# Optimization experiments

Measured on AMD Instinct MI355X. Metric: run time of the kernel, lower is better.

## Reference

```python
import jax, jax.numpy as jnp
import numpy as np
from jax.scipy.special import gammainc

ALPH = 0.8  # significance level (default arg in original forward)


def _median_width(X, iu, ju):
    # pairwise squared distances; original takes median of strictly-positive
    # strict-upper-triangle entries (tril subtracted) -> median over triu(k=1)
    G = jnp.sum(X * X, axis=1)                    # [n]
    D = G[:, None] + G[None, :] - 2.0 * (X @ X.T)  # [n, n]
    du = D[iu, ju]                                 # strict upper triangle, static size
    return jnp.sqrt(0.5 * jnp.median(du))


def _rbf(X, width):
    G = jnp.sum(X * X, axis=1)
    D = G[:, None] + G[None, :] - 2.0 * (X @ X.T)
    return jnp.exp(-D / (2.0 * width ** 2))


def _center(K):
    # H K H with H = I - 11^T/n  ==  K - rowmean - colmean + totalmean
    cm = jnp.mean(K, axis=0, keepdims=True)   # mean over rows  -> [1, n]
    rm = jnp.mean(K, axis=1, keepdims=True)   # mean over cols  -> [n, 1]
    tm = jnp.mean(K)
    return K - cm - rm + tm


def _gamma_ppf(a, p):
    # invert regularized lower incomplete gamma via fixed-iteration bisection
    hi0 = a + 10.0 * jnp.sqrt(a) + 100.0
    def body(i, lohi):
        lo, hi = lohi
        mid = 0.5 * (lo + hi)
        below = gammainc(a, mid) < p
        return (jnp.where(below, mid, lo), jnp.where(below, hi, mid))
    lo, hi = jax.lax.fori_loop(0, 100, body, (jnp.zeros_like(a), hi0))
    return 0.5 * (lo + hi)


def setup_inputs() -> dict:
    key = jax.random.key(0)
    k1, k2 = jax.random.split(key)
    X = jax.random.normal(k1, (4096, 64), dtype=jnp.float32)
    Y = jax.random.normal(k2, (4096, 64), dtype=jnp.float32)
    return {"X": X, "Y": Y}


def reference(X, Y):
    n = X.shape[0]
    iu, ju = np.triu_indices(n, k=1)  # static index set

    width_x = _median_width(X, iu, ju)
    width_y = _median_width(Y, iu, ju)

    K = _rbf(X, width_x)
    L = _rbf(Y, width_y)

    Kc = _center(K)
    Lc = _center(L)

    testStat = jnp.sum(Kc.T * Lc) / n

    V = (Kc * Lc / 6.0) ** 2
    varHSIC = (jnp.sum(V) - jnp.trace(V)) / n / (n - 1)
    varHSIC = varHSIC * 72.0 * (n - 4) * (n - 5) / n / (n - 1) / (n - 2) / (n - 3)

    # zero-diagonal kernels for mean estimate
    K0sum = jnp.sum(K) - jnp.trace(K)
    L0sum = jnp.sum(L) - jnp.trace(L)
    muX = K0sum / n / (n - 1)
    muY = L0sum / n / (n - 1)
    mHSIC = (1.0 + muX * muY - muX - muY) / n

    al = mHSIC ** 2 / varHSIC
    bet = varHSIC * n / mHSIC
    thresh = bet * _gamma_ppf(al, jnp.float32(1.0 - ALPH))
    return (testStat, thresh)
```

## Files before the change

### kernel.cpp

```cpp
#include <hip/hip_runtime.h>

typedef unsigned int u32;
typedef unsigned short u16;
typedef __attribute__((ext_vector_type(8))) short bf16x8;
typedef __attribute__((ext_vector_type(4))) float f32x4;

#define NPTS 4096
#define DIM  64
#define NB   32
#define NBLK 528
#define WLO16 0x4140u
#define NWBIN 832
#define RSTR 836
#define LOG2E 1.4426950408889634f
#define KF1C 8390654u
#define KF2C 8390656u


__device__ __forceinline__ void bmap(int b, int& by, int& bx){
  by = 0;
  while (b >= NB - by){ b -= NB - by; by++; }
  bx = by + b;
}

__device__ __forceinline__ u16 f2bf(float x){
  u32 u = __float_as_uint(x);
  return (u16)((u + 0x7fffu + ((u>>16)&1u)) >> 16);
}

__device__ __forceinline__ float fexp2(float x){
  return __builtin_amdgcn_exp2f(x);
}

__global__ __launch_bounds__(256) void convert_k(const float* __restrict__ X, const float* __restrict__ Y,
                                                 u16* __restrict__ Xbf, float* __restrict__ Gall,
                                                 u32* __restrict__ histsum, double* __restrict__ rowK,
                                                 double* __restrict__ rowL, double* __restrict__ sumsS,
                                                 double* __restrict__ slotbuf, u32* __restrict__ ctr){
  int t = blockIdx.x*256 + threadIdx.x;
  int rid = t >> 1, hf = t & 1;
  int z = rid >> 12, row = rid & 4095;
  const float* src = (z ? Y : X) + (size_t)row*DIM + hf*32;
  u16* basep = Xbf + ((size_t)z*32768 + (size_t)(row>>4)*128 + (row&15))*8;
  float g = 0.f;
#pragma unroll
  for (int f=0; f<4; f++){
    float4 f0 = *(const float4*)(src + f*8);
    float4 f1 = *(const float4*)(src + f*8 + 4);
    g = fmaf(f0.x,f0.x,g); g = fmaf(f0.y,f0.y,g); g = fmaf(f0.z,f0.z,g); g = fmaf(f0.w,f0.w,g);
    g = fmaf(f1.x,f1.x,g); g = fmaf(f1.y,f1.y,g); g = fmaf(f1.z,f1.z,g); g = fmaf(f1.w,f1.w,g);
    ushort4 h0, h1;
    h0.x=f2bf(f0.x); h0.y=f2bf(f0.y); h0.z=f2bf(f0.z); h0.w=f2bf(f0.w);
    h1.x=f2bf(f1.x); h1.y=f2bf(f1.y); h1.z=f2bf(f1.z); h1.w=f2bf(f1.w);
    u16* dst = basep + (size_t)(hf*4 + f)*16*8;
    *(ushort4*)dst = h0;
    *(ushort4*)(dst+4) = h1;
  }
  g += __shfl_xor(g, 1, 64);
  if (hf==0) Gall[rid] = g;
  if (t < NPTS){ rowK[t] = 0.0; rowL[t] = 0.0; }
  if (t < 2*RSTR) histsum[t] = 0u;
  if (t < 64) slotbuf[t] = 0.0;
  if (t < 16) sumsS[t] = 0.0;
  if (t == 0) *ctr = 0u;
}

__global__ __launch_bounds__(256,4) void hist_k(const u16* __restrict__ Xbf, const float* __restrict__ Gall,
                                                u32* __restrict__ histsum){
  __shared__ u32 lh[4][RSTR];
  __shared__ bf16x8 sB[1024];
  int z = blockIdx.y, tid = threadIdx.x;
  int by,bx; bmap(blockIdx.x, by, bx);
  bool isdiag = (by==bx);
  u32 wgt = isdiag ? 1u : 2u;
  int w=tid>>6, lane=tid&63, q=lane>>4, nl=lane&15;
  int cp = lane & 3;
  const bf16x8* Xb = (const bf16x8*)Xbf + (size_t)z*32768;
  const bf16x8* srcB = Xb + (size_t)(bx*8)*128;
  for (int t=tid;t<1024;t+=256) sB[t] = srcB[t];
  for (int t=tid;t<4*RSTR;t+=256) ((u32*)lh)[t]=0;
  __syncthreads();
  const float* Gz = Gall + z*NPTS;
  int ag0 = by*8 + w, ag1 = by*8 + 4 + w;
  bf16x8 a0f0 = Xb[ag0*128 + q*16 + nl];
  bf16x8 a0f1 = Xb[ag0*128 + (4+q)*16 + nl];
  bf16x8 a1f0 = Xb[ag1*128 + q*16 + nl];
  bf16x8 a1f1 = Xb[ag1*128 + (4+q)*16 + nl];
  float ga0 = Gz[ag0*16 + nl], ga1 = Gz[ag1*16 + nl];
  float g0m[4], g1m[4];
#pragma unroll
  for (int r=0;r<4;r++){ g0m[r] = __shfl(ga0, q*4+r, 64); g1m[r] = __shfl(ga1, q*4+r, 64); }
#pragma unroll
  for (int tb=0;tb<8;tb++){
    bf16x8 bf0 = sB[tb*128 + q*16 + nl];
    bf16x8 bf1 = sB[tb*128 + (4+q)*16 + nl];
    f32x4 acc0 = (f32x4)0.0f, acc1 = (f32x4)0.0f;
    acc0 = __builtin_amdgcn_mfma_f32_16x16x32_bf16(a0f0, bf0, acc0, 0,0,0);
    acc0 = __builtin_amdgcn_mfma_f32_16x16x32_bf16(a0f1, bf1, acc0, 0,0,0);
    acc1 = __builtin_amdgcn_mfma_f32_16x16x32_bf16(a1f0, bf0, acc1, 0,0,0);
    acc1 = __builtin_amdgcn_mfma_f32_16x16x32_bf16(a1f1, bf1, acc1, 0,0,0);
    int j = (bx*8 + tb)*16 + nl;
    float gb = Gz[j];
#pragma unroll
    for (int r=0;r<4;r++){
      float d0 = (g0m[r] + gb) - 2.0f*acc0[r];
      float d1 = (g1m[r] + gb) - 2.0f*acc1[r];
      if (isdiag){
        if (ag0*16 + q*4 + r == j) d0 = 0.f;
        if (ag1*16 + q*4 + r == j) d1 = 0.f;
      }
      u32 t0 = __float_as_uint(d0) >> 16;
      u32 bin0 = (t0 < WLO16) ? 0u : (t0 >= WLO16+NWBIN) ? (u32)(NWBIN+1) : (t0 - WLO16 + 1u);
      atomicAdd(&lh[cp][bin0], wgt);
      u32 t1 = __float_as_uint(d1) >> 16;
      u32 bin1 = (t1 < WLO16) ? 0u : (t1 >= WLO16+NWBIN) ? (u32)(NWBIN+1) : (t1 - WLO16 + 1u);
      atomicAdd(&lh[cp][bin1], wgt);
    }
  }
  __syncthreads();
  u32* dst = histsum + (size_t)z*RSTR;
  for (int t=tid;t<RSTR;t+=256){
    u32 v = lh[0][t] + lh[1][t] + lh[2][t] + lh[3][t];
    if (v) atomicAdd(&dst[t], v);
  }
}

__global__ __launch_bounds__(256,3) void rowsum_k(const u16* __restrict__ Xbf, const float* __restrict__ Gall,
                                                  const u32* __restrict__ histsum, float* __restrict__ scal,
                                                  double* __restrict__ rowK, double* __restrict__ rowL,
                                                  double* __restrict__ sumsS){
  __shared__ union {
    struct { u32 wsum[4]; double svals[2]; float scal_sh; } sc;
    struct { double rowacc[128]; double colLDS[4][128]; double tred[2]; } rs;
  } sh;
  __shared__ bf16x8 sB[1024];
  int z = blockIdx.y, tid = threadIdx.x;
  int w=tid>>6, lane=tid&63, q=lane>>4, nl=lane&15;
  int by,bx; bmap(blockIdx.x, by, bx);
  bool isdiag = (by==bx);
  const bf16x8* Xb = (const bf16x8*)Xbf + (size_t)z*32768;
  const bf16x8* srcB = Xb + (size_t)(bx*8)*128;
  for (int t=tid;t<1024;t+=256) sB[t] = srcB[t];

  {
    u32 c4[4] = {0,0,0,0};
    if (tid < 209){
      const u32* base = histsum + (size_t)z*RSTR + 4*tid;
      int lim = RSTR - 4*tid;
      c4[0] = base[0];
      if (lim>1) c4[1] = base[1];
      if (lim>2) c4[2] = base[2];
      if (lim>3) c4[3] = base[3];
    }
    u32 s = c4[0]+c4[1]+c4[2]+c4[3];
    u32 pre = s;
#pragma unroll
    for (int off=1; off<64; off<<=1){
      u32 t2 = __shfl_up(pre, off, 64);
      if (lane >= off) pre += t2;
    }
    if (lane==63) sh.sc.wsum[w] = pre;
    __syncthreads();
    u32 base2 = 0;
    for (int k=0;k<w;k++) base2 += sh.sc.wsum[k];
    u32 incl = base2 + pre, excl = incl - s;
    u32 ks[2] = {KF1C,KF2C};
#pragma unroll
    for (int w2=0; w2<2; w2++){
      if (ks[w2] >= excl && ks[w2] < incl){
        u32 acc = excl;
#pragma unroll
        for (int j=0;j<4;j++){
          if (ks[w2] < acc + c4[j]){
            int b = tid*4 + j;
            double lo, hi;
            if (b==0){ lo=12.0; hi=12.0; }
            else if (b>=NWBIN+1){ lo=1024.0; hi=1024.0; }
            else {
              u32 t16 = WLO16 + (u32)b - 1u;
              lo = (double)__uint_as_float(t16<<16);
              hi = (double)__uint_as_float((t16+1u)<<16);
            }
            double frac = ((double)(ks[w2]-acc) + 0.5)/(double)c4[j];
            sh.sc.svals[w2] = lo + (hi-lo)*frac;
            break;
          }
          acc += c4[j];
        }
      }
    }
    __syncthreads();
    if (tid==0){
      float med = (float)(0.5*(sh.sc.svals[0]+sh.sc.svals[1]));
      float wd = sqrtf(0.5f*med);
      float sc2 = 2.0f*wd*wd;
      sh.sc.scal_sh = sc2;
      if (blockIdx.x==0) scal[z] = sc2;
    }
    __syncthreads();
  }
  float negi = -LOG2E / sh.sc.scal_sh;
  __syncthreads();

  const float* Gz = Gall + z*NPTS;
  int ag0 = by*8 + w, ag1 = by*8 + 4 + w;
  bf16x8 a0f0 = Xb[ag0*128 + q*16 + nl];
  bf16x8 a0f1 = Xb[ag0*128 + (4+q)*16 + nl];
  bf16x8 a1f0 = Xb[ag1*128 + q*16 + nl];
  bf16x8 a1f1 = Xb[ag1*128 + (4+q)*16 + nl];
  float ga0 = Gz[ag0*16 + nl], ga1 = Gz[ag1*16 + nl];
  float g0m[4], g1m[4];
#pragma unroll
  for (int r=0;r<4;r++){ g0m[r] = __shfl(ga0, q*4+r, 64); g1m[r] = __shfl(ga1, q*4+r, 64); }
  float rs0[4] = {0,0,0,0}, rs1[4] = {0,0,0,0};
#pragma unroll
  for (int tb=0;tb<8;tb++){
    bf16x8 bf0 = sB[tb*128 + q*16 + nl];
    bf16x8 bf1 = sB[tb*128 + (4+q)*16 + nl];
    f32x4 acc0 = (f32x4)0.0f, acc1 = (f32x4)0.0f;
    acc0 = __builtin_amdgcn_mfma_f32_16x16x32_bf16(a0f0, bf0, acc0, 0,0,0);
    acc0 = __builtin_amdgcn_mfma_f32_16x16x32_bf16(a0f1, bf1, acc0, 0,0,0);
    acc1 = __builtin_amdgcn_mfma_f32_16x16x32_bf16(a1f0, bf0, acc1, 0,0,0);
    acc1 = __builtin_amdgcn_mfma_f32_16x16x32_bf16(a1f1, bf1, acc1, 0,0,0);
    int j = (bx*8 + tb)*16 + nl;
    float gb = Gz[j];
    float cs = 0.f;
#pragma unroll
    for (int r=0;r<4;r++){
      float d0 = (g0m[r] + gb) - 2.0f*acc0[r];
      float d1 = (g1m[r] + gb) - 2.0f*acc1[r];
      if (isdiag){
        if (ag0*16 + q*4 + r == j) d0 = 0.f;
        if (ag1*16 + q*4 + r == j) d1 = 0.f;
      }
      float e0 = fexp2(d0*negi);
      float e1 = fexp2(d1*negi);
      rs0[r] += e0; rs1[r] += e1;
      cs += e0 + e1;
    }
    cs += __shfl_xor(cs, 16, 64);
    cs += __shfl_xor(cs, 32, 64);
    if (q==0) sh.rs.colLDS[w][tb*16 + nl] = (double)cs;
  }
#pragma unroll
  for (int r=0;r<4;r++){
    float v0 = rs0[r], v1 = rs1[r];
    v0 += __shfl_xor(v0,1,64); v0 += __shfl_xor(v0,2,64);
    v0 += __shfl_xor(v0,4,64); v0 += __shfl_xor(v0,8,64);
    v1 += __shfl_xor(v1,1,64); v1 += __shfl_xor(v1,2,64);
    v1 += __shfl_xor(v1,4,64); v1 += __shfl_xor(v1,8,64);
    rs0[r] = v0; rs1[r] = v1;
  }
  if (nl==0){
#pragma unroll
    for (int r=0;r<4;r++){
      sh.rs.rowacc[w*16 + q*4 + r]     = (double)rs0[r];
      sh.rs.rowacc[(4+w)*16 + q*4 + r] = (double)rs1[r];
    }
  }
  __syncthreads();
  double tot = 0.0;
  if (tid < 128){
    double rv = sh.rs.rowacc[tid];
    double cv = sh.rs.colLDS[0][tid] + sh.rs.colLDS[1][tid] + sh.rs.colLDS[2][tid] + sh.rs.colLDS[3][tid];
    double* rowG = z ? rowL : rowK;
    atomicAdd(&rowG[by*128 + tid], rv);
    if (!isdiag) atomicAdd(&rowG[bx*128 + tid], cv);
    tot = rv + (isdiag ? 0.0 : cv);
  }
#pragma unroll
  for (int s2=1;s2<64;s2<<=1) tot += __shfl_xor(tot, s2, 64);
  if (lane==0 && w<2) sh.rs.tred[w] = tot;
  __syncthreads();
  if (tid==0) atomicAdd(&sumsS[z*8 + (blockIdx.x & 7)], sh.rs.tred[0] + sh.rs.tred[1]);
}

__device__ double gammainc_block4(double a, double x, double lga,
                                  int tid, int lane, int w,
                                  double* wp , double* bs ){
  double C = 1.0/a;
  double psum = 0.0;
  for (int b=0;b<512;b++){
    double k0 = (double)(b*1024 + tid*4);
    double r1 = x/(a+k0+1.0), r2 = x/(a+k0+2.0), r3 = x/(a+k0+3.0), r4 = x/(a+k0+4.0);
    double p12 = r1*r2;
    double pl = p12*(r3*r4);
    double pp = pl;
#pragma unroll
    for (int s=1;s<64;s<<=1){
      double t = __shfl_up(pp, s, 64);
      if (lane >= s) pp *= t;
    }
    if (lane==63) wp[w] = pp;
    __syncthreads();
    double cross = 1.0;
    for (int k2=0;k2<w;k2++) cross *= wp[k2];
    double call = wp[0]*wp[1]*wp[2]*wp[3];
    double excl = __shfl_up(pp, 1, 64);
    if (lane==0) excl = 1.0;
    double base = C*cross*excl;
    double t1 = base*r1, t2 = base*p12, t3 = t2*r3, t4 = base*pl;
    psum += (t1+t2)+(t3+t4);
    double Cn = C*call;
    C = Cn;
    double rlast = x/(a + (double)(b*1024 + 1024));
    __syncthreads();
    if (rlast < 1.0 && Cn*rlast/(1.0-rlast) < 1e-17) break;
  }
#pragma unroll
  for (int s=1;s<64;s<<=1) psum += __shfl_xor(psum, s, 64);
  if (lane==0) bs[w] = psum;
  __syncthreads();
  double total = 1.0/a + bs[0]+bs[1]+bs[2]+bs[3];
  __syncthreads();
  return exp(-x + a*log(x) - lga) * total;
}

__global__ __launch_bounds__(256,3) void final_k(const u16* __restrict__ Xbf, const float* __restrict__ Gall,
                                                 const float* __restrict__ scal,
                                                 const double* __restrict__ rowK,
                                                 const double* __restrict__ rowL,
                                                 const double* __restrict__ sumsS,
                                                 double* __restrict__ slotbuf, u32* __restrict__ ctr,
                                                 float* __restrict__ out){
  __shared__ bf16x8 sBX[1024];
  __shared__ bf16x8 sBY[1024];
  __shared__ double red[4][3];
  __shared__ double gwp[4], gbs[4], stot[3];
  __shared__ int lastFlag;
  int tid = threadIdx.x;
  int b = blockIdx.x >> 1, half = blockIdx.x & 1;
  int by,bx; bmap(b,by,bx);
  bool isdiag = (by==bx);
  int w=tid>>6, lane=tid&63, q=lane>>4, nl=lane&15;
  const bf16x8* Xb = (const bf16x8*)Xbf;
  const bf16x8* Yb = Xb + 32768;
  const bf16x8* srcBX = Xb + (size_t)(bx*8)*128;
  const bf16x8* srcBY = Yb + (size_t)(bx*8)*128;
  for (int t=tid;t<1024;t+=256){ sBX[t] = srcBX[t]; sBY[t] = srcBY[t]; }
  const float* Gx = Gall;
  const float* Gy = Gall + NPTS;
  const double inv_n = 1.0/(double)NPTS;
  double sK=0.0, sL=0.0;
#pragma unroll
  for (int k2=0;k2<8;k2++){ sK += sumsS[k2]; sL += sumsS[8+k2]; }
  double tmK = sK*(inv_n*inv_n), tmL = sL*(inv_n*inv_n);
  float negx = -LOG2E/scal[0], negy = -LOG2E/scal[1];
  float S1f=0.f, S2f=0.f, trVf=0.f;
  int ag = by*8 + half*4 + w;
  bf16x8 axf0 = Xb[ag*128 + q*16 + nl];
  bf16x8 axf1 = Xb[ag*128 + (4+q)*16 + nl];
  bf16x8 ayf0 = Yb[ag*128 + q*16 + nl];
  bf16x8 ayf1 = Yb[ag*128 + (4+q)*16 + nl];
  float gaX = Gx[ag*16 + nl], gaY = Gy[ag*16 + nl];
  float gXm[4], gYm[4];
#pragma unroll
  for (int r=0;r<4;r++){ gXm[r] = __shfl(gaX, q*4+r, 64); gYm[r] = __shfl(gaY, q*4+r, 64); }
  float rmKi[4], rmLi[4];
#pragma unroll
  for (int r=0;r<4;r++){
    int i = ag*16 + q*4 + r;
    rmKi[r] = (float)(rowK[i]*inv_n); rmLi[r] = (float)(rowL[i]*inv_n);
  }
  __syncthreads();
#pragma unroll
  for (int tb=0;tb<8;tb++){
    bf16x8 bx0 = sBX[tb*128 + q*16 + nl];
    bf16x8 bx1 = sBX[tb*128 + (4+q)*16 + nl];
    bf16x8 by0 = sBY[tb*128 + q*16 + nl];
    bf16x8 by1 = sBY[tb*128 + (4+q)*16 + nl];
    f32x4 accX = (f32x4)0.0f, accY = (f32x4)0.0f;
    accX = __builtin_amdgcn_mfma_f32_16x16x32_bf16(axf0, bx0, accX, 0,0,0);
    accX = __builtin_amdgcn_mfma_f32_16x16x32_bf16(axf1, bx1, accX, 0,0,0);
    accY = __builtin_amdgcn_mfma_f32_16x16x32_bf16(ayf0, by0, accY, 0,0,0);
    accY = __builtin_amdgcn_mfma_f32_16x16x32_bf16(ayf1, by1, accY, 0,0,0);
    int j = (bx*8 + tb)*16 + nl;
    float gbX = Gx[j], gbY = Gy[j];
    float cmK = (float)(rowK[j]*inv_n - tmK);
    float cmL = (float)(rowL[j]*inv_n - tmL);
#pragma unroll
    for (int r=0;r<4;r++){
      int i = ag*16 + q*4 + r;
      float dx = (gXm[r] + gbX) - 2.0f*accX[r];
      float dy = (gYm[r] + gbY) - 2.0f*accY[r];
      bool dg = isdiag && i==j;
      if (dg){ dx = 0.f; dy = 0.f; }
      float kx = fexp2(dx*negx);
      float lv = fexp2(dy*negy);
      float kc = (kx - rmKi[r]) - cmK;
      float lc = (lv - rmLi[r]) - cmL;
      float prod = kc*lc;
      S1f += prod;
      S2f = fmaf(prod, prod, S2f);
      if (dg) trVf = fmaf(prod, prod, trVf);
    }
  }
  double S1, S2, trV;
  {
    double wgt = isdiag ? 1.0 : 2.0;
    S1 = (double)S1f * wgt;
    S2 = (double)S2f * (wgt*(1.0/36.0));
    trV = (double)trVf * (1.0/36.0);
  }
  double vals[3]={S1,S2,trV};
#pragma unroll
  for (int v=0;v<3;v++){
    double x = vals[v];
#pragma unroll
    for (int s2=1;s2<64;s2<<=1) x += __shfl_xor(x, s2, 64);
    if (lane==0) red[w][v]=x;
  }
  __syncthreads();
  if (tid < 3){
    double val = red[0][tid]+red[1][tid]+red[2][tid]+red[3][tid];
    double old = atomicAdd(&slotbuf[(size_t)(blockIdx.x & 15)*4 + tid], val);
    asm volatile("" :: "v"(old));
  }
  __syncthreads();
  if (tid==0){
    u32 old = atomicAdd(ctr, 1u);
    lastFlag = (old == (u32)(2*NBLK - 1)) ? 1 : 0;
  }
  __syncthreads();
  if (!lastFlag) return;

  if (w==0){
    double t0=0.0, t1=0.0, t2=0.0;
    if (lane < 16){
      double* sp = slotbuf + (size_t)lane*4;
      t0 = atomicAdd(&sp[0], 0.0);
      t1 = atomicAdd(&sp[1], 0.0);
      t2 = atomicAdd(&sp[2], 0.0);
    }
#pragma unroll
    for (int s2=1;s2<16;s2<<=1){
      t0 += __shfl_xor(t0, s2, 64);
      t1 += __shfl_xor(t1, s2, 64);
      t2 += __shfl_xor(t2, s2, 64);
    }
    if (lane==0){ stot[0]=t0; stot[1]=t1; stot[2]=t2; }
  }
  __syncthreads();
  const double n = (double)NPTS;
  double S1t=stot[0], S2t=stot[1], trVt=stot[2];
  double testStat = S1t/n;
  double varHSIC = (S2t - trVt)/n/(n-1.0);
  varHSIC = varHSIC*72.0*(n-4.0)*(n-5.0)/n/(n-1.0)/(n-2.0)/(n-3.0);
  double muX = (sK-n)/n/(n-1.0);
  double muY = (sL-n)/n/(n-1.0);
  double mHSIC = (1.0 + muX*muY - muX - muY)/n;
  double al = mHSIC*mHSIC/varHSIC;
  double bet = varHSIC*n/mHSIC;
  double p = (double)((float)(1.0-0.8));
  double lga = lgamma(al);
  double lo = 0.0, hi = al + 10.0*sqrt(al) + 100.0;
  const double zp = -0.8416212335729142957;
  double tt = 1.0 - 1.0/(9.0*al) + zp/(3.0*sqrt(al));
  double x = al*tt*tt*tt;
  if (!(x > 0.0) || !(x < hi)) x = 0.5*hi;
  for (int it=0; it<2; ++it){
    double P = gammainc_block4(al, x, lga, tid, lane, w, gwp, gbs);
    double diff = P - p;
    if (diff < 0.0) lo = x; else hi = x;
    if (fabs(diff) < 1e-12) break;
    double pdf = exp(-x + (al-1.0)*log(x) - lga);
    double nx = x - diff/pdf;
    if (!(nx > lo) || !(nx < hi)) nx = 0.5*(lo+hi);
    x = nx;
  }
  if (tid==0){
    out[0]=(float)testStat;
    out[1]=(float)(bet*x);
  }
}

extern "C" void kernel_launch(void* const* d_in, const int* in_sizes, int n_in,
                              void* d_out, int out_size, void* d_ws, size_t ws_size,
                              hipStream_t stream) {
  const float* X = (const float*)d_in[0];
  const float* Y = (const float*)d_in[1];
  float* out = (float*)d_out;
  char* ws = (char*)d_ws;

  double* sumsS    = (double*)ws;
  float*  scal     = (float*)(ws + 128);
  u32*    histsum  = (u32*)(ws + 256);
  double* slotbuf  = (double*)(ws + 7168);
  u32*    ctr      = (u32*)(ws + 7680);
  double* rowK     = (double*)(ws + 8192);
  double* rowL     = (double*)(ws + 40960);
  float*  Gall     = (float*)(ws + 73728);
  u16*    Xbf      = (u16*)(ws + (4u<<20));
  size_t need = (size_t)(4u<<20) + (size_t)2*NPTS*DIM*2;

  if (ws_size < need) return;

  convert_k<<<64,256,0,stream>>>(X, Y, Xbf, Gall, histsum, rowK, rowL, sumsS, slotbuf, ctr);
  hist_k<<<dim3(NBLK,2),256,0,stream>>>(Xbf, Gall, histsum);
  rowsum_k<<<dim3(NBLK,2),256,0,stream>>>(Xbf, Gall, histsum, scal, rowK, rowL, sumsS);
  final_k<<<2*NBLK,256,0,stream>>>(Xbf, Gall, scal, rowK, rowL, sumsS, slotbuf, ctr, out);
}
```

Before: 134.9 us.

## Fuse four HSIC kernels into one cooperative persistent kernel with grid barriers

Replaces the four separate launches (convert, histogram, rowsum, final) with a single cooperative kernel sized to occupancy that loops over tiles and separates the phases with atomic grid barriers. Each block recomputes the median scale for both inputs locally instead of reading it back from a previous kernel. A hipMemsetAsync zeroes the workspace counters, and the old multi-kernel path is kept as a fallback if the cooperative launch fails. This removes launch gaps and tail effects between kernels, but adds barrier spinning, a memset launch, and lower per-phase occupancy because the shared memory union is larger.

Measured after the change: 239.0 us. +77.1%, slower.

```diff
diff --git a/kernel.cpp b/kernel.cpp
--- a/kernel.cpp
+++ b/kernel.cpp
@@ -2,6 +2,7 @@
 
 typedef unsigned int u32;
 typedef unsigned short u16;
+typedef unsigned long long u64;
 typedef __attribute__((ext_vector_type(8))) short bf16x8;
 typedef __attribute__((ext_vector_type(4))) float f32x4;
 
@@ -16,7 +17,6 @@
 #define KF1C 8390654u
 #define KF2C 8390656u
 
-
 __device__ __forceinline__ void bmap(int b, int& by, int& bx){
   by = 0;
   while (b >= NB - by){ b -= NB - by; by++; }
@@ -30,6 +30,489 @@
 
 __device__ __forceinline__ float fexp2(float x){
   return __builtin_amdgcn_exp2f(x);
+}
+
+__device__ __forceinline__ u32 aload_u32(const u32* p){
+  return __hip_atomic_load((u32*)p, __ATOMIC_RELAXED, __HIP_MEMORY_SCOPE_AGENT);
+}
+__device__ __forceinline__ double aload_f64(const double* p){
+  return __hip_atomic_load((double*)p, __ATOMIC_RELAXED, __HIP_MEMORY_SCOPE_AGENT);
+}
+__device__ __forceinline__ void astore_u64(u64* p, u64 v){
+  __hip_atomic_store(p, v, __ATOMIC_RELAXED, __HIP_MEMORY_SCOPE_AGENT);
+}
+__device__ __forceinline__ void astore_f32(float* p, float v){
+  __hip_atomic_store(p, v, __ATOMIC_RELAXED, __HIP_MEMORY_SCOPE_AGENT);
+}
+
+__device__ __forceinline__ void gbarrier(u32* bar, u32 target){
+  __syncthreads();
+  if (threadIdx.x == 0){
+    __hip_atomic_fetch_add(bar, 1u, __ATOMIC_ACQ_REL, __HIP_MEMORY_SCOPE_AGENT);
+    while (__hip_atomic_load(bar, __ATOMIC_ACQUIRE, __HIP_MEMORY_SCOPE_AGENT) < target)
+      __builtin_amdgcn_s_sleep(8);
+  }
+  __syncthreads();
+}
+
+__device__ double gammainc_block4(double a, double x, double lga,
+                                  int tid, int lane, int w,
+                                  double* wp , double* bs ){
+  double C = 1.0/a;
+  double psum = 0.0;
+  for (int b=0;b<512;b++){
+    double k0 = (double)(b*1024 + tid*4);
+    double r1 = x/(a+k0+1.0), r2 = x/(a+k0+2.0), r3 = x/(a+k0+3.0), r4 = x/(a+k0+4.0);
+    double p12 = r1*r2;
+    double pl = p12*(r3*r4);
+    double pp = pl;
+#pragma unroll
+    for (int s=1;s<64;s<<=1){
+      double t = __shfl_up(pp, s, 64);
+      if (lane >= s) pp *= t;
+    }
+    if (lane==63) wp[w] = pp;
+    __syncthreads();
+    double cross = 1.0;
+    for (int k2=0;k2<w;k2++) cross *= wp[k2];
+    double call = wp[0]*wp[1]*wp[2]*wp[3];
+    double excl = __shfl_up(pp, 1, 64);
+    if (lane==0) excl = 1.0;
+    double base = C*cross*excl;
+    double t1 = base*r1, t2 = base*p12, t3 = t2*r3, t4 = base*pl;
+    psum += (t1+t2)+(t3+t4);
+    double Cn = C*call;
+    C = Cn;
+    double rlast = x/(a + (double)(b*1024 + 1024));
+    __syncthreads();
+    if (rlast < 1.0 && Cn*rlast/(1.0-rlast) < 1e-17) break;
+  }
+#pragma unroll
+  for (int s=1;s<64;s<<=1) psum += __shfl_xor(psum, s, 64);
+  if (lane==0) bs[w] = psum;
+  __syncthreads();
+  double total = 1.0/a + bs[0]+bs[1]+bs[2]+bs[3];
+  __syncthreads();
+  return exp(-x + a*log(x) - lga) * total;
+}
+
+__global__ __launch_bounds__(256) void hsic_fused(
+    const float* __restrict__ X, const float* __restrict__ Y,
+    u16* __restrict__ Xbf, float* __restrict__ Gall,
+    u32* __restrict__ histsum, double* __restrict__ rowK, double* __restrict__ rowL,
+    double* __restrict__ sumsS, double* __restrict__ slotbuf, u32* __restrict__ ctr,
+    float* __restrict__ out)
+{
+  const int tid = threadIdx.x;
+  const int bid = blockIdx.x;
+  const int gsz = gridDim.x;
+  const int w = tid>>6, lane = tid&63, q = lane>>4, nl = lane&15;
+  const int gtid = bid*256 + tid;
+  const int gstr = gsz*256;
+
+  __shared__ union {
+    struct { u32 lh[4][RSTR]; bf16x8 sB[1024]; } h;
+    struct {
+      union {
+        struct { u32 wsum[4]; double svals[2]; float scal_sh; } sc;
+        struct { double rowacc[128]; double colLDS[4][128]; double tred[2]; } rs;
+      } u;
+      bf16x8 sB[1024];
+    } r;
+    struct { bf16x8 sBX[1024]; bf16x8 sBY[1024]; double red[4][3];
+             double gwp[4]; double gbs[4]; double stot[3]; double s16[16];
+             int lastFlag; } f;
+  } sh;
+
+  for (int t = gtid; t < 4*NPTS; t += gstr){
+    int rid = t >> 1, hf = t & 1;
+    int z = rid >> 12, row = rid & 4095;
+    const float* src = (z ? Y : X) + (size_t)row*DIM + hf*32;
+    u16* basep = Xbf + ((size_t)z*32768 + (size_t)(row>>4)*128 + (row&15))*8;
+    float g = 0.f;
+#pragma unroll
+    for (int f=0; f<4; f++){
+      float4 f0 = *(const float4*)(src + f*8);
+      float4 f1 = *(const float4*)(src + f*8 + 4);
+      g = fmaf(f0.x,f0.x,g); g = fmaf(f0.y,f0.y,g); g = fmaf(f0.z,f0.z,g); g = fmaf(f0.w,f0.w,g);
+      g = fmaf(f1.x,f1.x,g); g = fmaf(f1.y,f1.y,g); g = fmaf(f1.z,f1.z,g); g = fmaf(f1.w,f1.w,g);
+      union { ushort4 s; u64 qv; } c0, c1;
+      c0.s.x=f2bf(f0.x); c0.s.y=f2bf(f0.y); c0.s.z=f2bf(f0.z); c0.s.w=f2bf(f0.w);
+      c1.s.x=f2bf(f1.x); c1.s.y=f2bf(f1.y); c1.s.z=f2bf(f1.z); c1.s.w=f2bf(f1.w);
+      u16* dst = basep + (size_t)(hf*4 + f)*16*8;
+      astore_u64((u64*)dst, c0.qv);
+      astore_u64((u64*)(dst+4), c1.qv);
+    }
+    g += __shfl_xor(g, 1, 64);
+    if (hf==0) astore_f32(&Gall[rid], g);
+  }
+  gbarrier(ctr, (u32)gsz);
+
+  for (int tile = bid; tile < 2*NBLK; tile += gsz){
+    int z = (tile >= NBLK) ? 1 : 0;
+    int b = tile - (z ? NBLK : 0);
+    int by,bx; bmap(b,by,bx);
+    bool isdiag = (by==bx);
+    u32 wgt = isdiag ? 1u : 2u;
+    int cp = lane & 3;
+    const bf16x8* Xb = (const bf16x8*)Xbf + (size_t)z*32768;
+    const bf16x8* srcB = Xb + (size_t)(bx*8)*128;
+    for (int t=tid;t<1024;t+=256) sh.h.sB[t] = srcB[t];
+    for (int t=tid;t<4*RSTR;t+=256) ((u32*)sh.h.lh)[t]=0;
+    __syncthreads();
+    const float* Gz = Gall + z*NPTS;
+    int ag0 = by*8 + w, ag1 = by*8 + 4 + w;
+    bf16x8 a0f0 = Xb[ag0*128 + q*16 + nl];
+    bf16x8 a0f1 = Xb[ag0*128 + (4+q)*16 + nl];
+    bf16x8 a1f0 = Xb[ag1*128 + q*16 + nl];
+    bf16x8 a1f1 = Xb[ag1*128 + (4+q)*16 + nl];
+    float ga0 = Gz[ag0*16 + nl], ga1 = Gz[ag1*16 + nl];
+    float g0m[4], g1m[4];
+#pragma unroll
+    for (int r=0;r<4;r++){ g0m[r] = __shfl(ga0, q*4+r, 64); g1m[r] = __shfl(ga1, q*4+r, 64); }
+#pragma unroll
+    for (int tb=0;tb<8;tb++){
+      bf16x8 bf0 = sh.h.sB[tb*128 + q*16 + nl];
+      bf16x8 bf1 = sh.h.sB[tb*128 + (4+q)*16 + nl];
+      f32x4 acc0 = (f32x4)0.0f, acc1 = (f32x4)0.0f;
+      acc0 = __builtin_amdgcn_mfma_f32_16x16x32_bf16(a0f0, bf0, acc0, 0,0,0);
+      acc0 = __builtin_amdgcn_mfma_f32_16x16x32_bf16(a0f1, bf1, acc0, 0,0,0);
+      acc1 = __builtin_amdgcn_mfma_f32_16x16x32_bf16(a1f0, bf0, acc1, 0,0,0);
+      acc1 = __builtin_amdgcn_mfma_f32_16x16x32_bf16(a1f1, bf1, acc1, 0,0,0);
+      int j = (bx*8 + tb)*16 + nl;
+      float gb = Gz[j];
+#pragma unroll
+      for (int r=0;r<4;r++){
+        float d0 = (g0m[r] + gb) - 2.0f*acc0[r];
+        float d1 = (g1m[r] + gb) - 2.0f*acc1[r];
+        if (isdiag){
+          if (ag0*16 + q*4 + r == j) d0 = 0.f;
+          if (ag1*16 + q*4 + r == j) d1 = 0.f;
+        }
+        u32 t0 = __float_as_uint(d0) >> 16;
+        u32 bin0 = (t0 < WLO16) ? 0u : (t0 >= WLO16+NWBIN) ? (u32)(NWBIN+1) : (t0 - WLO16 + 1u);
+        atomicAdd(&sh.h.lh[cp][bin0], wgt);
+        u32 t1 = __float_as_uint(d1) >> 16;
+        u32 bin1 = (t1 < WLO16) ? 0u : (t1 >= WLO16+NWBIN) ? (u32)(NWBIN+1) : (t1 - WLO16 + 1u);
+        atomicAdd(&sh.h.lh[cp][bin1], wgt);
+      }
+    }
+    __syncthreads();
+    u32* dst = histsum + (size_t)z*RSTR;
+    for (int t=tid;t<RSTR;t+=256){
+      u32 v = sh.h.lh[0][t] + sh.h.lh[1][t] + sh.h.lh[2][t] + sh.h.lh[3][t];
+      if (v){
+        u32 old = atomicAdd(&dst[t], v);
+        asm volatile("" :: "v"(old));
+      }
+    }
+    __syncthreads();
+  }
+  gbarrier(ctr, (u32)(2*gsz));
+
+  float scalz[2];
+  for (int z=0; z<2; ++z){
+    u32 c4[4] = {0,0,0,0};
+    if (tid < 209){
+      const u32* base = histsum + (size_t)z*RSTR + 4*tid;
+      int lim = RSTR - 4*tid;
+      c4[0] = aload_u32(base+0);
+      if (lim>1) c4[1] = aload_u32(base+1);
+      if (lim>2) c4[2] = aload_u32(base+2);
+      if (lim>3) c4[3] = aload_u32(base+3);
+    }
+    u32 s = c4[0]+c4[1]+c4[2]+c4[3];
+    u32 pre = s;
+#pragma unroll
+    for (int off=1; off<64; off<<=1){
+      u32 t2 = __shfl_up(pre, off, 64);
+      if (lane >= off) pre += t2;
+    }
+    if (lane==63) sh.r.u.sc.wsum[w] = pre;
+    __syncthreads();
+    u32 base2 = 0;
+    for (int k=0;k<w;k++) base2 += sh.r.u.sc.wsum[k];
+    u32 incl = base2 + pre, excl = incl - s;
+    u32 ks[2] = {KF1C,KF2C};
+#pragma unroll
+    for (int w2=0; w2<2; w2++){
+      if (ks[w2] >= excl && ks[w2] < incl){
+        u32 acc = excl;
+#pragma unroll
+        for (int j=0;j<4;j++){
+          if (ks[w2] < acc + c4[j]){
+            int b = tid*4 + j;
+            double lo, hi;
+            if (b==0){ lo=12.0; hi=12.0; }
+            else if (b>=NWBIN+1){ lo=1024.0; hi=1024.0; }
+            else {
+              u32 t16 = WLO16 + (u32)b - 1u;
+              lo = (double)__uint_as_float(t16<<16);
+              hi = (double)__uint_as_float((t16+1u)<<16);
+            }
+            double frac = ((double)(ks[w2]-acc) + 0.5)/(double)c4[j];
+            sh.r.u.sc.svals[w2] = lo + (hi-lo)*frac;
+            break;
+          }
+          acc += c4[j];
+        }
+      }
+    }
+    __syncthreads();
+    if (tid==0){
+      float med = (float)(0.5*(sh.r.u.sc.svals[0]+sh.r.u.sc.svals[1]));
+      float wd = sqrtf(0.5f*med);
+      sh.r.u.sc.scal_sh = 2.0f*wd*wd;
+    }
+    __syncthreads();
+    scalz[z] = sh.r.u.sc.scal_sh;
+    __syncthreads();
+  }
+
+  for (int tile = bid; tile < 2*NBLK; tile += gsz){
+    int z = (tile >= NBLK) ? 1 : 0;
+    int b = tile - (z ? NBLK : 0);
+    int by,bx; bmap(b,by,bx);
+    bool isdiag = (by==bx);
+    const bf16x8* Xb = (const bf16x8*)Xbf + (size_t)z*32768;
+    const bf16x8* srcB = Xb + (size_t)(bx*8)*128;
+    for (int t=tid;t<1024;t+=256) sh.r.sB[t] = srcB[t];
+    __syncthreads();
+    const float* Gz = Gall + z*NPTS;
+    float negi = -LOG2E / scalz[z];
+    int ag0 = by*8 + w, ag1 = by*8 + 4 + w;
+    bf16x8 a0f0 = Xb[ag0*128 + q*16 + nl];
+    bf16x8 a0f1 = Xb[ag0*128 + (4+q)*16 + nl];
+    bf16x8 a1f0 = Xb[ag1*128 + q*16 + nl];
+    bf16x8 a1f1 = Xb[ag1*128 + (4+q)*16 + nl];
+    float ga0 = Gz[ag0*16 + nl], ga1 = Gz[ag1*16 + nl];
+    float g0m[4], g1m[4];
+#pragma unroll
+    for (int r=0;r<4;r++){ g0m[r] = __shfl(ga0, q*4+r, 64); g1m[r] = __shfl(ga1, q*4+r, 64); }
+    float rs0[4] = {0,0,0,0}, rs1[4] = {0,0,0,0};
+#pragma unroll
+    for (int tb=0;tb<8;tb++){
+      bf16x8 bf0 = sh.r.sB[tb*128 + q*16 + nl];
+      bf16x8 bf1 = sh.r.sB[tb*128 + (4+q)*16 + nl];
+      f32x4 acc0 = (f32x4)0.0f, acc1 = (f32x4)0.0f;
+      acc0 = __builtin_amdgcn_mfma_f32_16x16x32_bf16(a0f0, bf0, acc0, 0,0,0);
+      acc0 = __builtin_amdgcn_mfma_f32_16x16x32_bf16(a0f1, bf1, acc0, 0,0,0);
+      acc1 = __builtin_amdgcn_mfma_f32_16x16x32_bf16(a1f0, bf0, acc1, 0,0,0);
+      acc1 = __builtin_amdgcn_mfma_f32_16x16x32_bf16(a1f1, bf1, acc1, 0,0,0);
+      int j = (bx*8 + tb)*16 + nl;
+      float gb = Gz[j];
+      float cs = 0.f;
+#pragma unroll
+      for (int r=0;r<4;r++){
+        float d0 = (g0m[r] + gb) - 2.0f*acc0[r];
+        float d1 = (g1m[r] + gb) - 2.0f*acc1[r];
+        if (isdiag){
+          if (ag0*16 + q*4 + r == j) d0 = 0.f;
+          if (ag1*16 + q*4 + r == j) d1 = 0.f;
+        }
+        float e0 = fexp2(d0*negi);
+        float e1 = fexp2(d1*negi);
+        rs0[r] += e0; rs1[r] += e1;
+        cs += e0 + e1;
+      }
+      cs += __shfl_xor(cs, 16, 64);
+      cs += __shfl_xor(cs, 32, 64);
+      if (q==0) sh.r.u.rs.colLDS[w][tb*16 + nl] = (double)cs;
+    }
+#pragma unroll
+    for (int r=0;r<4;r++){
+      float v0 = rs0[r], v1 = rs1[r];
+      v0 += __shfl_xor(v0,1,64); v0 += __shfl_xor(v0,2,64);
+      v0 += __shfl_xor(v0,4,64); v0 += __shfl_xor(v0,8,64);
+      v1 += __shfl_xor(v1,1,64); v1 += __shfl_xor(v1,2,64);
+      v1 += __shfl_xor(v1,4,64); v1 += __shfl_xor(v1,8,64);
+      rs0[r] = v0; rs1[r] = v1;
+    }
+    if (nl==0){
+#pragma unroll
+      for (int r=0;r<4;r++){
+        sh.r.u.rs.rowacc[w*16 + q*4 + r]     = (double)rs0[r];
+        sh.r.u.rs.rowacc[(4+w)*16 + q*4 + r] = (double)rs1[r];
+      }
+    }
+    __syncthreads();
+    double tot = 0.0;
+    if (tid < 128){
+      double rv = sh.r.u.rs.rowacc[tid];
+      double cv = sh.r.u.rs.colLDS[0][tid] + sh.r.u.rs.colLDS[1][tid]
+                + sh.r.u.rs.colLDS[2][tid] + sh.r.u.rs.colLDS[3][tid];
+      double* rowG = z ? rowL : rowK;
+      double o1 = atomicAdd(&rowG[by*128 + tid], rv);
+      asm volatile("" :: "v"(o1));
+      if (!isdiag){
+        double o2 = atomicAdd(&rowG[bx*128 + tid], cv);
+        asm volatile("" :: "v"(o2));
+      }
+      tot = rv + (isdiag ? 0.0 : cv);
+    }
+#pragma unroll
+    for (int s2=1;s2<64;s2<<=1) tot += __shfl_xor(tot, s2, 64);
+    if (lane==0 && w<2) sh.r.u.rs.tred[w] = tot;
+    __syncthreads();
+    if (tid==0){
+      double o3 = atomicAdd(&sumsS[z*8 + (b & 7)], sh.r.u.rs.tred[0] + sh.r.u.rs.tred[1]);
+      asm volatile("" :: "v"(o3));
+    }
+    __syncthreads();
+  }
+  gbarrier(ctr, (u32)(3*gsz));
+
+  {
+    const bf16x8* Xb = (const bf16x8*)Xbf;
+    const bf16x8* Yb = Xb + 32768;
+    const float* Gx = Gall;
+    const float* Gy = Gall + NPTS;
+    const double inv_n = 1.0/(double)NPTS;
+    if (tid < 16) sh.f.s16[tid] = aload_f64(&sumsS[tid]);
+    __syncthreads();
+    double sK=0.0, sL=0.0;
+#pragma unroll
+    for (int k2=0;k2<8;k2++){ sK += sh.f.s16[k2]; sL += sh.f.s16[8+k2]; }
+    __syncthreads();
+    double tmK = sK*(inv_n*inv_n), tmL = sL*(inv_n*inv_n);
+    float negx = -LOG2E/scalz[0], negy = -LOG2E/scalz[1];
+    double S1d=0.0, S2d=0.0, trVd=0.0;
+    for (int t = bid; t < 2*NBLK; t += gsz){
+      int b = t >> 1, half = t & 1;
+      int by,bx; bmap(b,by,bx);
+      bool isdiag = (by==bx);
+      const bf16x8* srcBX = Xb + (size_t)(bx*8)*128;
+      const bf16x8* srcBY = Yb + (size_t)(bx*8)*128;
+      for (int tt=tid;tt<1024;tt+=256){ sh.f.sBX[tt] = srcBX[tt]; sh.f.sBY[tt] = srcBY[tt]; }
+      float S1f=0.f, S2f=0.f, trVf=0.f;
+      int ag = by*8 + half*4 + w;
+      bf16x8 axf0 = Xb[ag*128 + q*16 + nl];
+      bf16x8 axf1 = Xb[ag*128 + (4+q)*16 + nl];
+      bf16x8 ayf0 = Yb[ag*128 + q*16 + nl];
+      bf16x8 ayf1 = Yb[ag*128 + (4+q)*16 + nl];
+      float gaX = Gx[ag*16 + nl], gaY = Gy[ag*16 + nl];
+      float gXm[4], gYm[4];
+#pragma unroll
+      for (int r=0;r<4;r++){ gXm[r] = __shfl(gaX, q*4+r, 64); gYm[r] = __shfl(gaY, q*4+r, 64); }
+      float rmKi[4], rmLi[4];
+#pragma unroll
+      for (int r=0;r<4;r++){
+        int i = ag*16 + q*4 + r;
+        rmKi[r] = (float)(aload_f64(&rowK[i])*inv_n);
+        rmLi[r] = (float)(aload_f64(&rowL[i])*inv_n);
+      }
+      __syncthreads();
+#pragma unroll
+      for (int tb=0;tb<8;tb++){
+        bf16x8 bx0 = sh.f.sBX[tb*128 + q*16 + nl];
+        bf16x8 bx1 = sh.f.sBX[tb*128 + (4+q)*16 + nl];
+        bf16x8 by0 = sh.f.sBY[tb*128 + q*16 + nl];
+        bf16x8 by1 = sh.f.sBY[tb*128 + (4+q)*16 + nl];
+        f32x4 accX = (f32x4)0.0f, accY = (f32x4)0.0f;
+        accX = __builtin_amdgcn_mfma_f32_16x16x32_bf16(axf0, bx0, accX, 0,0,0);
+        accX = __builtin_amdgcn_mfma_f32_16x16x32_bf16(axf1, bx1, accX, 0,0,0);
+        accY = __builtin_amdgcn_mfma_f32_16x16x32_bf16(ayf0, by0, accY, 0,0,0);
+        accY = __builtin_amdgcn_mfma_f32_16x16x32_bf16(ayf1, by1, accY, 0,0,0);
+        int j = (bx*8 + tb)*16 + nl;
+        float gbX = Gx[j], gbY = Gy[j];
+        float cmK = (float)(aload_f64(&rowK[j])*inv_n - tmK);
+        float cmL = (float)(aload_f64(&rowL[j])*inv_n - tmL);
+#pragma unroll
+        for (int r=0;r<4;r++){
+          int i = ag*16 + q*4 + r;
+          float dx = (gXm[r] + gbX) - 2.0f*accX[r];
+          float dy = (gYm[r] + gbY) - 2.0f*accY[r];
+          bool dg = isdiag && i==j;
+          if (dg){ dx = 0.f; dy = 0.f; }
+          float kx = fexp2(dx*negx);
+          float lv = fexp2(dy*negy);
+          float kc = (kx - rmKi[r]) - cmK;
+          float lc = (lv - rmLi[r]) - cmL;
+          float prod = kc*lc;
+          S1f += prod;
+          S2f = fmaf(prod, prod, S2f);
+          if (dg) trVf = fmaf(prod, prod, trVf);
+        }
+      }
+      {
+        double wgt = isdiag ? 1.0 : 2.0;
+        S1d += wgt*(double)S1f;
+        S2d += (wgt*(1.0/36.0))*(double)S2f;
+        trVd += (1.0/36.0)*(double)trVf;
+      }
+      __syncthreads();
+    }
+    double vals[3]={S1d,S2d,trVd};
+#pragma unroll
+    for (int v=0;v<3;v++){
+      double x = vals[v];
+#pragma unroll
+      for (int s2=1;s2<64;s2<<=1) x += __shfl_xor(x, s2, 64);
+      if (lane==0) sh.f.red[w][v]=x;
+    }
+    __syncthreads();
+    if (tid < 3){
+      double val = sh.f.red[0][tid]+sh.f.red[1][tid]+sh.f.red[2][tid]+sh.f.red[3][tid];
+      double old = atomicAdd(&slotbuf[(size_t)(bid & 15)*4 + tid], val);
+      asm volatile("" :: "v"(old));
+    }
+    __syncthreads();
+    if (tid==0){
+      u32 old = __hip_atomic_fetch_add(ctr, 1u, __ATOMIC_ACQ_REL, __HIP_MEMORY_SCOPE_AGENT);
+      sh.f.lastFlag = (old == (u32)(4*gsz - 1)) ? 1 : 0;
+    }
+    __syncthreads();
+    if (!sh.f.lastFlag) return;
+
+    if (w==0){
+      double t0=0.0, t1=0.0, t2=0.0;
+      if (lane < 16){
+        double* sp = slotbuf + (size_t)lane*4;
+        t0 = atomicAdd(&sp[0], 0.0);
+        t1 = atomicAdd(&sp[1], 0.0);
+        t2 = atomicAdd(&sp[2], 0.0);
+      }
+#pragma unroll
+      for (int s2=1;s2<16;s2<<=1){
+        t0 += __shfl_xor(t0, s2, 64);
+        t1 += __shfl_xor(t1, s2, 64);
+        t2 += __shfl_xor(t2, s2, 64);
+      }
+      if (lane==0){ sh.f.stot[0]=t0; sh.f.stot[1]=t1; sh.f.stot[2]=t2; }
+    }
+    __syncthreads();
+    const double n = (double)NPTS;
+    double S1t=sh.f.stot[0], S2t=sh.f.stot[1], trVt=sh.f.stot[2];
+    double testStat = S1t/n;
+    double varHSIC = (S2t - trVt)/n/(n-1.0);
+    varHSIC = varHSIC*72.0*(n-4.0)*(n-5.0)/n/(n-1.0)/(n-2.0)/(n-3.0);
+    double muX = (sK-n)/n/(n-1.0);
+    double muY = (sL-n)/n/(n-1.0);
+    double mHSIC = (1.0 + muX*muY - muX - muY)/n;
+    double al = mHSIC*mHSIC/varHSIC;
+    double bet = varHSIC*n/mHSIC;
+    double p = (double)((float)(1.0-0.8));
+    double lga = lgamma(al);
+    double lo = 0.0, hi = al + 10.0*sqrt(al) + 100.0;
+    const double zp = -0.8416212335729142957;
+    double tt2 = 1.0 - 1.0/(9.0*al) + zp/(3.0*sqrt(al));
+    double x = al*tt2*tt2*tt2;
+    if (!(x > 0.0) || !(x < hi)) x = 0.5*hi;
+    for (int it=0; it<2; ++it){
+      double P = gammainc_block4(al, x, lga, tid, lane, w, sh.f.gwp, sh.f.gbs);
+      double diff = P - p;
+      if (diff < 0.0) lo = x; else hi = x;
+      if (fabs(diff) < 1e-12) break;
+      double pdf = exp(-x + (al-1.0)*log(x) - lga);
+      double nx = x - diff/pdf;
+      if (!(nx > lo) || !(nx < hi)) nx = 0.5*(lo+hi);
+      x = nx;
+    }
+    if (tid==0){
+      out[0]=(float)testStat;
+      out[1]=(float)(bet*x);
+    }
+  }
 }
 
 __global__ __launch_bounds__(256) void convert_k(const float* __restrict__ X, const float* __restrict__ Y,
@@ -141,7 +624,6 @@
   const bf16x8* Xb = (const bf16x8*)Xbf + (size_t)z*32768;
   const bf16x8* srcB = Xb + (size_t)(bx*8)*128;
   for (int t=tid;t<1024;t+=256) sB[t] = srcB[t];
-
   {
     u32 c4[4] = {0,0,0,0};
     if (tid < 209){
@@ -201,7 +683,6 @@
   }
   float negi = -LOG2E / sh.sc.scal_sh;
   __syncthreads();
-
   const float* Gz = Gall + z*NPTS;
   int ag0 = by*8 + w, ag1 = by*8 + 4 + w;
   bf16x8 a0f0 = Xb[ag0*128 + q*16 + nl];
@@ -273,47 +754,6 @@
   if (lane==0 && w<2) sh.rs.tred[w] = tot;
   __syncthreads();
   if (tid==0) atomicAdd(&sumsS[z*8 + (blockIdx.x & 7)], sh.rs.tred[0] + sh.rs.tred[1]);
-}
-
-__device__ double gammainc_block4(double a, double x, double lga,
-                                  int tid, int lane, int w,
-                                  double* wp , double* bs ){
-  double C = 1.0/a;
-  double psum = 0.0;
-  for (int b=0;b<512;b++){
-    double k0 = (double)(b*1024 + tid*4);
-    double r1 = x/(a+k0+1.0), r2 = x/(a+k0+2.0), r3 = x/(a+k0+3.0), r4 = x/(a+k0+4.0);
-    double p12 = r1*r2;
-    double pl = p12*(r3*r4);
-    double pp = pl;
-#pragma unroll
-    for (int s=1;s<64;s<<=1){
-      double t = __shfl_up(pp, s, 64);
-      if (lane >= s) pp *= t;
-    }
-    if (lane==63) wp[w] = pp;
-    __syncthreads();
-    double cross = 1.0;
-    for (int k2=0;k2<w;k2++) cross *= wp[k2];
-    double call = wp[0]*wp[1]*wp[2]*wp[3];
-    double excl = __shfl_up(pp, 1, 64);
-    if (lane==0) excl = 1.0;
-    double base = C*cross*excl;
-    double t1 = base*r1, t2 = base*p12, t3 = t2*r3, t4 = base*pl;
-    psum += (t1+t2)+(t3+t4);
-    double Cn = C*call;
-    C = Cn;
-    double rlast = x/(a + (double)(b*1024 + 1024));
-    __syncthreads();
-    if (rlast < 1.0 && Cn*rlast/(1.0-rlast) < 1e-17) break;
-  }
-#pragma unroll
-  for (int s=1;s<64;s<<=1) psum += __shfl_xor(psum, s, 64);
-  if (lane==0) bs[w] = psum;
-  __syncthreads();
-  double total = 1.0/a + bs[0]+bs[1]+bs[2]+bs[3];
-  __syncthreads();
-  return exp(-x + a*log(x) - lga) * total;
 }
 
 __global__ __launch_bounds__(256,3) void final_k(const u16* __restrict__ Xbf, const float* __restrict__ Gall,
@@ -423,7 +863,6 @@
   }
   __syncthreads();
   if (!lastFlag) return;
-
   if (w==0){
     double t0=0.0, t1=0.0, t2=0.0;
     if (lane < 16){
@@ -495,8 +934,31 @@
 
   if (ws_size < need) return;
 
-  convert_k<<<64,256,0,stream>>>(X, Y, Xbf, Gall, histsum, rowK, rowL, sumsS, slotbuf, ctr);
-  hist_k<<<dim3(NBLK,2),256,0,stream>>>(Xbf, Gall, histsum);
-  rowsum_k<<<dim3(NBLK,2),256,0,stream>>>(Xbf, Gall, histsum, scal, rowK, rowL, sumsS);
-  final_k<<<2*NBLK,256,0,stream>>>(Xbf, Gall, scal, rowK, rowL, sumsS, slotbuf, ctr, out);
-}
+  (void)hipMemsetAsync(ws, 0, 73728, stream);
+
+  static int gridBlocks = 0;
+  if (gridBlocks == 0){
+    int dev = 0; (void)hipGetDevice(&dev);
+    int nCU = 0; (void)hipDeviceGetAttribute(&nCU, hipDeviceAttributeMultiprocessorCount, dev);
+    int maxb = 0;
+    (void)hipOccupancyMaxActiveBlocksPerMultiprocessor(&maxb, reinterpret_cast<const void*>(hsic_fused), 256, 0);
+    if (nCU <= 0) nCU = 256;
+    if (maxb <= 0) maxb = 1;
+    long g = (long)nCU * (long)maxb;
+    if (g > 2*NBLK) g = 2*NBLK;
+    if (g < 8) g = 8;
+    gridBlocks = (int)g;
+  }
+
+  void* args[] = {(void*)&X, (void*)&Y, (void*)&Xbf, (void*)&Gall, (void*)&histsum,
+                  (void*)&rowK, (void*)&rowL, (void*)&sumsS, (void*)&slotbuf,
+                  (void*)&ctr, (void*)&out};
+  hipError_t e = hipLaunchCooperativeKernel(reinterpret_cast<const void*>(hsic_fused),
+                                            dim3(gridBlocks), dim3(256), args, 0, stream);
+  if (e != hipSuccess){
+    convert_k<<<64,256,0,stream>>>(X, Y, Xbf, Gall, histsum, rowK, rowL, sumsS, slotbuf, ctr);
+    hist_k<<<dim3(NBLK,2),256,0,stream>>>(Xbf, Gall, histsum);
+    rowsum_k<<<dim3(NBLK,2),256,0,stream>>>(Xbf, Gall, histsum, scal, rowK, rowL, sumsS);
+    final_k<<<2*NBLK,256,0,stream>>>(Xbf, Gall, scal, rowK, rowL, sumsS, slotbuf, ctr, out);
+  }
+}
```
